# Kernel tuning notes

Hardware: AMD Instinct MI355X
Metric: run time of the kernel (lower is better)

Reference implementation:

```python
import jax, jax.numpy as jnp
import numpy as np

G = 8192   # number of groups / clusters of samples
S = 64     # samples per group
N = G * S
D = 128
H = 256
K = 8      # n_clusters
EPS = 0.01


def setup_inputs() -> dict:
    key = jax.random.key(0)
    ks = jax.random.split(key, 6)
    index = jnp.repeat(jnp.arange(G, dtype=jnp.int32), S)  # sorted, contiguous groups
    x = jax.random.normal(ks[0], (N, D), dtype=jnp.float32)
    y = jax.random.normal(ks[1], (N, 1), dtype=jnp.float32)
    anchor_x = jax.random.normal(ks[2], (G, D), dtype=jnp.float32)
    anchor_y = jax.random.normal(ks[3], (G, 1), dtype=jnp.float32)
    W1 = jax.random.normal(ks[4], (D, H), dtype=jnp.float32) / np.sqrt(D)
    b1 = jnp.zeros((H,), jnp.float32)
    W2 = jax.random.normal(ks[5], (H, K + 2), dtype=jnp.float32) / np.sqrt(H)
    b2 = jnp.zeros((K + 2,), jnp.float32)
    return {"index": index, "x": x, "y": y, "anchor_x": anchor_x,
            "anchor_y": anchor_y, "W1": W1, "b1": b1, "W2": W2, "b2": b2}


def reference(index, x, y, anchor_x, anchor_y, W1, b1, W2, b2):
    idx = index
    # repeat_interleave(anchor, sizes) == gather for sorted contiguous index
    x_rel = x - anchor_x[idx]            # [N, D]
    y_rel = y - anchor_y[idx]            # [N, 1]

    seg = lambda v: jax.ops.segment_sum(v, idx, num_segments=G)
    n = seg(jnp.ones((x.shape[0], 1), x.dtype))          # [G, 1] group sizes
    sx = seg(x_rel)                                       # [G, D]
    sy = seg(y_rel)                                       # [G, 1]
    sxy = seg(x_rel * y_rel)                              # [G, D]
    # per-group unbiased cross-covariance cov(x, y)
    cov = (sxy - sx * sy / n) / (n - 1.0)                 # [G, D]

    # per-group scalar variance of x_rel flattened over [n_g, D] (torch .var())
    sxx = seg((x_rel * x_rel).sum(-1, keepdims=True))     # [G, 1]
    tot = sx.sum(-1, keepdims=True)                       # [G, 1]
    nD = n * x.shape[1]
    var = (sxx - tot * tot / nD) / (nD - 1.0)             # [G, 1]

    rep = cov / var                                       # xtxinv * representation

    # MLP head (Tanh hidden, dropout is identity at inference)
    h = jnp.tanh(rep @ W1 + b1)
    out = h @ W2 + b2                                     # [G, K+2]
    alpha = jax.nn.softplus(out[:, :1]) * (1.0 - EPS) + EPS
    beta = jax.nn.softplus(out[:, 1:2]) * (1.0 - EPS) + EPS
    mixture = jax.nn.softmax(out[:, 2:], axis=-1)         # [G, K]
    scale = jnp.sqrt(beta / alpha)                        # sqrt(1/precision_mean)
    # Gamma(alpha, beta) / Categorical(mixture) returned via their parameters
    return (rep, mixture, scale, alpha, beta)
```

## Files before the change

### kernel.cpp

```cpp
#include <hip/hip_runtime.h>
#include <math.h>

#define NG   8192
#define NS   64
#define ND   128
#define NH   256
#define NO   10
#define GPB  16

__global__ __launch_bounds__(256) void stats_kernel(
    const float* __restrict__ x, const float* __restrict__ y,
    const float* __restrict__ ax, const float* __restrict__ ay,
    float* __restrict__ rep)
{
    const int g = blockIdx.x;
    const int t = threadIdx.x;
    const int c = t & 31;
    const int r = t >> 5;

    __shared__ float  yL[NS];
    __shared__ float4 axL[32];
    __shared__ float4 sxL[8][32];
    __shared__ float4 sxyL[8][32];
    __shared__ float  sxxL[256];

    if (t < NS) {
        yL[t] = y[g * NS + t] - ay[g];
    } else if (t < NS + 32) {
        axL[t - NS] = ((const float4*)ax)[g * 32 + (t - NS)];
    }
    __syncthreads();

    const float4 a4 = axL[c];
    const float4* xg = (const float4*)x + (size_t)g * (NS * 32) + r * (8 * 32) + c;

    float sx0 = 0.f, sx1 = 0.f, sx2 = 0.f, sx3 = 0.f;
    float sy0 = 0.f, sy1 = 0.f, sy2 = 0.f, sy3 = 0.f;
    float sxx = 0.f;
#pragma unroll
    for (int i = 0; i < 8; ++i) {
        float4 xv = xg[i * 32];
        float yr = yL[r * 8 + i];
        float x0 = xv.x - a4.x;
        float x1 = xv.y - a4.y;
        float x2 = xv.z - a4.z;
        float x3 = xv.w - a4.w;
        sx0 += x0; sx1 += x1; sx2 += x2; sx3 += x3;
        sy0 += x0 * yr; sy1 += x1 * yr; sy2 += x2 * yr; sy3 += x3 * yr;
        sxx += x0 * x0 + x1 * x1 + x2 * x2 + x3 * x3;
    }
    sxL[r][c]  = make_float4(sx0, sx1, sx2, sx3);
    sxyL[r][c] = make_float4(sy0, sy1, sy2, sy3);
    sxxL[t] = sxx;
    __syncthreads();

    if (t < 32) {
        float4 sxv  = sxL[0][t];
        float4 sxyv = sxyL[0][t];
        float  sxxs = sxxL[t];
#pragma unroll
        for (int rr = 1; rr < 8; ++rr) {
            float4 a = sxL[rr][t];
            float4 b = sxyL[rr][t];
            sxv.x += a.x; sxv.y += a.y; sxv.z += a.z; sxv.w += a.w;
            sxyv.x += b.x; sxyv.y += b.y; sxyv.z += b.z; sxyv.w += b.w;
            sxxs += sxxL[rr * 32 + t];
        }
        float tot = sxv.x + sxv.y + sxv.z + sxv.w;
        float sy  = yL[t] + yL[t + 32];
#pragma unroll
        for (int off = 16; off >= 1; off >>= 1) {
            tot  += __shfl_xor(tot, off);
            sxxs += __shfl_xor(sxxs, off);
            sy   += __shfl_xor(sy, off);
        }
        float var = (sxxs - tot * tot * (1.0f / 8192.0f)) * (1.0f / 8191.0f);
        float iv = 1.0f / var;
        float c0 = sy * (1.0f / 64.0f);
        float4 rp;
        rp.x = (sxyv.x - sxv.x * c0) * (1.0f / 63.0f) * iv;
        rp.y = (sxyv.y - sxv.y * c0) * (1.0f / 63.0f) * iv;
        rp.z = (sxyv.z - sxv.z * c0) * (1.0f / 63.0f) * iv;
        rp.w = (sxyv.w - sxv.w * c0) * (1.0f / 63.0f) * iv;
        ((float4*)rep)[g * 32 + t] = rp;
    }
}

__device__ __forceinline__ float fast_tanh(float v) {
    v = fminf(15.0f, fmaxf(-15.0f, v));
    float e = __expf(2.0f * v);
    return (e - 1.0f) / (e + 1.0f);
}

__device__ __forceinline__ float softplus_f(float v) {
    if (v > 15.0f) return v;
    return log1pf(__expf(v));
}

__global__ __launch_bounds__(256) void mlp_kernel(
    const float* __restrict__ rep, const float* __restrict__ W1,
    const float* __restrict__ b1, const float* __restrict__ W2,
    const float* __restrict__ b2, float* __restrict__ mix,
    float* __restrict__ scl, float* __restrict__ alp,
    float* __restrict__ bet)
{
    const int g0 = blockIdx.x * GPB;
    const int t = threadIdx.x;

    __shared__ __align__(16) float repL[GPB][ND];
    __shared__ float hL[GPB][NH + 1];
    __shared__ float w2L[NH * NO];
    __shared__ float outL[GPB][NO];

    {
        const float4* rp4 = (const float4*)(rep + (size_t)g0 * ND);
        float4* dst = (float4*)&repL[0][0];
        dst[t] = rp4[t];
        dst[t + 256] = rp4[t + 256];
    }
    for (int i = t; i < NH * NO; i += 256) w2L[i] = W2[i];
    __syncthreads();

    float acc[GPB];
#pragma unroll
    for (int g = 0; g < GPB; ++g) acc[g] = 0.f;

    for (int d = 0; d < ND; d += 4) {
        float w0 = W1[(d + 0) * NH + t];
        float w1 = W1[(d + 1) * NH + t];
        float w2 = W1[(d + 2) * NH + t];
        float w3 = W1[(d + 3) * NH + t];
#pragma unroll
        for (int g = 0; g < GPB; ++g) {
            const float4 r4 = *(const float4*)&repL[g][d];
            acc[g] += r4.x * w0 + r4.y * w1 + r4.z * w2 + r4.w * w3;
        }
    }
    const float bb = b1[t];
#pragma unroll
    for (int g = 0; g < GPB; ++g) {
        hL[g][t] = fast_tanh(acc[g] + bb);
    }
    __syncthreads();

    if (t < GPB * NO) {
        const int g = t / NO;
        const int k = t - g * NO;
        float s = b2[k];
#pragma unroll 8
        for (int j = 0; j < NH; ++j) s += hL[g][j] * w2L[j * NO + k];
        outL[g][k] = s;
    }
    __syncthreads();

    if (t < GPB) {
        const int gg = g0 + t;
        float al = softplus_f(outL[t][0]) * 0.99f + 0.01f;
        float be = softplus_f(outL[t][1]) * 0.99f + 0.01f;
        float m = -1e30f;
#pragma unroll
        for (int k = 0; k < 8; ++k) m = fmaxf(m, outL[t][2 + k]);
        float e[8];
        float sum = 0.f;
#pragma unroll
        for (int k = 0; k < 8; ++k) { e[k] = __expf(outL[t][2 + k] - m); sum += e[k]; }
        float inv = 1.0f / sum;
#pragma unroll
        for (int k = 0; k < 8; ++k) mix[gg * 8 + k] = e[k] * inv;
        alp[gg] = al;
        bet[gg] = be;
        scl[gg] = sqrtf(be / al);
    }
}

extern "C" void kernel_launch(void* const* d_in, const int* in_sizes, int n_in,
                              void* d_out, int out_size, void* d_ws, size_t ws_size,
                              hipStream_t stream) {
    const float* x  = (const float*)d_in[1];
    const float* y  = (const float*)d_in[2];
    const float* ax = (const float*)d_in[3];
    const float* ay = (const float*)d_in[4];
    const float* W1 = (const float*)d_in[5];
    const float* b1 = (const float*)d_in[6];
    const float* W2 = (const float*)d_in[7];
    const float* b2 = (const float*)d_in[8];

    float* out = (float*)d_out;
    float* rep = out;
    float* mix = out + (size_t)NG * ND;
    float* scl = mix + (size_t)NG * 8;
    float* alp = scl + NG;
    float* bet = alp + NG;

    stats_kernel<<<NG, 256, 0, stream>>>(x, y, ax, ay, rep);
    mlp_kernel<<<NG / GPB, 256, 0, stream>>>(rep, W1, b1, W2, b2, mix, scl, alp, bet);
}
```

Measured before the change: 401.6 us.

## Map one wavefront per group in stats kernel with shuffle-only reduction

Restructures the statistics kernel so each 64-lane wavefront handles one group, with four groups per block, instead of one 256-thread block per group. Each lane now issues batches of eight float4 loads to keep more memory requests in flight. The per-group reductions use cross-lane shuffles instead of shared-memory staging and block barriers. This relies on a shared-memory write being visible to other lanes of the same wavefront without a barrier, and it raises per-thread register use.

```diff
diff --git a/kernel.cpp b/kernel.cpp
--- a/kernel.cpp
+++ b/kernel.cpp
@@ -7,83 +7,73 @@
 #define NH   256
 #define NO   10
 #define GPB  16
+#define WPB  4
 
 __global__ __launch_bounds__(256) void stats_kernel(
     const float* __restrict__ x, const float* __restrict__ y,
     const float* __restrict__ ax, const float* __restrict__ ay,
     float* __restrict__ rep)
 {
-    const int g = blockIdx.x;
-    const int t = threadIdx.x;
-    const int c = t & 31;
-    const int r = t >> 5;
+    const int t    = threadIdx.x;
+    const int w    = t >> 6;
+    const int l    = t & 63;
+    const int g    = blockIdx.x * WPB + w;
+    const int c    = l & 31;
+    const int half = l >> 5;
 
-    __shared__ float  yL[NS];
-    __shared__ float4 axL[32];
-    __shared__ float4 sxL[8][32];
-    __shared__ float4 sxyL[8][32];
-    __shared__ float  sxxL[256];
+    __shared__ float yrelL[WPB][NS];
 
-    if (t < NS) {
-        yL[t] = y[g * NS + t] - ay[g];
-    } else if (t < NS + 32) {
-        axL[t - NS] = ((const float4*)ax)[g * 32 + (t - NS)];
+    float yv = y[g * NS + l] - ay[g];
+    yrelL[w][l] = yv;
+
+    const float4 a4 = ((const float4*)ax)[g * 32 + c];
+    const float4* xg = (const float4*)x
+                     + (size_t)g * (NS * 32) + (size_t)(half * 32) * 32 + c;
+
+    float4 sx  = make_float4(0.f, 0.f, 0.f, 0.f);
+    float4 sxy = make_float4(0.f, 0.f, 0.f, 0.f);
+    float  sxx = 0.f;
+
+#pragma unroll
+    for (int ii = 0; ii < 4; ++ii) {
+        float4 xv[8];
+#pragma unroll
+        for (int j = 0; j < 8; ++j) xv[j] = xg[(ii * 8 + j) * 32];
+#pragma unroll
+        for (int j = 0; j < 8; ++j) {
+            const float yr = yrelL[w][half * 32 + ii * 8 + j];
+            const float x0 = xv[j].x - a4.x;
+            const float x1 = xv[j].y - a4.y;
+            const float x2 = xv[j].z - a4.z;
+            const float x3 = xv[j].w - a4.w;
+            sx.x += x0; sx.y += x1; sx.z += x2; sx.w += x3;
+            sxy.x += x0 * yr; sxy.y += x1 * yr; sxy.z += x2 * yr; sxy.w += x3 * yr;
+            sxx += x0 * x0 + x1 * x1 + x2 * x2 + x3 * x3;
+        }
     }
-    __syncthreads();
 
-    const float4 a4 = axL[c];
-    const float4* xg = (const float4*)x + (size_t)g * (NS * 32) + r * (8 * 32) + c;
+    float tl = sx.x + sx.y + sx.z + sx.w;
+#pragma unroll
+    for (int off = 32; off >= 1; off >>= 1) {
+        tl  += __shfl_xor(tl,  off);
+        sxx += __shfl_xor(sxx, off);
+        yv  += __shfl_xor(yv,  off);
+    }
 
-    float sx0 = 0.f, sx1 = 0.f, sx2 = 0.f, sx3 = 0.f;
-    float sy0 = 0.f, sy1 = 0.f, sy2 = 0.f, sy3 = 0.f;
-    float sxx = 0.f;
-#pragma unroll
-    for (int i = 0; i < 8; ++i) {
-        float4 xv = xg[i * 32];
-        float yr = yL[r * 8 + i];
-        float x0 = xv.x - a4.x;
-        float x1 = xv.y - a4.y;
-        float x2 = xv.z - a4.z;
-        float x3 = xv.w - a4.w;
-        sx0 += x0; sx1 += x1; sx2 += x2; sx3 += x3;
-        sy0 += x0 * yr; sy1 += x1 * yr; sy2 += x2 * yr; sy3 += x3 * yr;
-        sxx += x0 * x0 + x1 * x1 + x2 * x2 + x3 * x3;
-    }
-    sxL[r][c]  = make_float4(sx0, sx1, sx2, sx3);
-    sxyL[r][c] = make_float4(sy0, sy1, sy2, sy3);
-    sxxL[t] = sxx;
-    __syncthreads();
+    sx.x  += __shfl_xor(sx.x,  32); sx.y  += __shfl_xor(sx.y,  32);
+    sx.z  += __shfl_xor(sx.z,  32); sx.w  += __shfl_xor(sx.w,  32);
+    sxy.x += __shfl_xor(sxy.x, 32); sxy.y += __shfl_xor(sxy.y, 32);
+    sxy.z += __shfl_xor(sxy.z, 32); sxy.w += __shfl_xor(sxy.w, 32);
 
-    if (t < 32) {
-        float4 sxv  = sxL[0][t];
-        float4 sxyv = sxyL[0][t];
-        float  sxxs = sxxL[t];
-#pragma unroll
-        for (int rr = 1; rr < 8; ++rr) {
-            float4 a = sxL[rr][t];
-            float4 b = sxyL[rr][t];
-            sxv.x += a.x; sxv.y += a.y; sxv.z += a.z; sxv.w += a.w;
-            sxyv.x += b.x; sxyv.y += b.y; sxyv.z += b.z; sxyv.w += b.w;
-            sxxs += sxxL[rr * 32 + t];
-        }
-        float tot = sxv.x + sxv.y + sxv.z + sxv.w;
-        float sy  = yL[t] + yL[t + 32];
-#pragma unroll
-        for (int off = 16; off >= 1; off >>= 1) {
-            tot  += __shfl_xor(tot, off);
-            sxxs += __shfl_xor(sxxs, off);
-            sy   += __shfl_xor(sy, off);
-        }
-        float var = (sxxs - tot * tot * (1.0f / 8192.0f)) * (1.0f / 8191.0f);
-        float iv = 1.0f / var;
-        float c0 = sy * (1.0f / 64.0f);
-        float4 rp;
-        rp.x = (sxyv.x - sxv.x * c0) * (1.0f / 63.0f) * iv;
-        rp.y = (sxyv.y - sxv.y * c0) * (1.0f / 63.0f) * iv;
-        rp.z = (sxyv.z - sxv.z * c0) * (1.0f / 63.0f) * iv;
-        rp.w = (sxyv.w - sxv.w * c0) * (1.0f / 63.0f) * iv;
-        ((float4*)rep)[g * 32 + t] = rp;
-    }
+    const float var = (sxx - tl * tl * (1.0f / 8192.0f)) * (1.0f / 8191.0f);
+    const float iv  = 1.0f / var;
+    const float c0  = yv * (1.0f / 64.0f);
+    float4 rp;
+    rp.x = (sxy.x - sx.x * c0) * (1.0f / 63.0f) * iv;
+    rp.y = (sxy.y - sx.y * c0) * (1.0f / 63.0f) * iv;
+    rp.z = (sxy.z - sx.z * c0) * (1.0f / 63.0f) * iv;
+    rp.w = (sxy.w - sx.w * c0) * (1.0f / 63.0f) * iv;
+    if (half == 0) ((float4*)rep)[g * 32 + c] = rp;
 }
 
 __device__ __forceinline__ float fast_tanh(float v) {
@@ -192,6 +182,6 @@
     float* alp = scl + NG;
     float* bet = alp + NG;
 
-    stats_kernel<<<NG, 256, 0, stream>>>(x, y, ax, ay, rep);
+    stats_kernel<<<NG / WPB, 256, 0, stream>>>(x, y, ax, ay, rep);
     mlp_kernel<<<NG / GPB, 256, 0, stream>>>(rep, W1, b1, W2, b2, mix, scl, alp, bet);
 }
```

Result: no change. 400.0 us (-0.4%).
